# Kernel optimization log

Hardware: AMD Instinct MI355X
Metric: run time of the kernel (lower is better)

The kernel has to match this reference:

```python
import jax, jax.numpy as jnp
import numpy as np

VOCAB = 14
EMBED = 10
HIDDEN = 50
MLP = 50
PAD_IDX = 0
BATCH = 4096
SEQ = 2048


def setup_inputs() -> dict:
    key = jax.random.key(0)
    ks = jax.random.split(key, 10)
    tokens = jax.random.randint(ks[0], (BATCH, SEQ), 0, VOCAB, dtype=jnp.int64 if jax.config.jax_enable_x64 else jnp.int32)
    s_lstm = 1.0 / np.sqrt(HIDDEN)
    s_mlp1 = 1.0 / np.sqrt(HIDDEN)
    s_mlp2 = 1.0 / np.sqrt(MLP)
    emb = jax.random.normal(ks[1], (VOCAB, EMBED), jnp.float32)
    emb = emb.at[PAD_IDX].set(0.0)  # padding_idx row is zero in torch Embedding
    W_ih = jax.random.uniform(ks[2], (4 * HIDDEN, EMBED), jnp.float32, -s_lstm, s_lstm)
    W_hh = jax.random.uniform(ks[3], (4 * HIDDEN, HIDDEN), jnp.float32, -s_lstm, s_lstm)
    b_ih = jax.random.uniform(ks[4], (4 * HIDDEN,), jnp.float32, -s_lstm, s_lstm)
    b_hh = jax.random.uniform(ks[5], (4 * HIDDEN,), jnp.float32, -s_lstm, s_lstm)
    W1 = jax.random.uniform(ks[6], (MLP, HIDDEN), jnp.float32, -s_mlp1, s_mlp1)
    b1 = jax.random.uniform(ks[7], (MLP,), jnp.float32, -s_mlp1, s_mlp1)
    W2 = jax.random.uniform(ks[8], (1, MLP), jnp.float32, -s_mlp2, s_mlp2)
    b2 = jax.random.uniform(ks[9], (1,), jnp.float32, -s_mlp2, s_mlp2)
    return {"input": tokens, "emb": emb, "W_ih": W_ih, "W_hh": W_hh,
            "b_ih": b_ih, "b_hh": b_hh, "W1": W1, "b1": b1, "W2": W2, "b2": b2}


def reference(input, emb, W_ih, W_hh, b_ih, b_hh, W1, b1, W2, b2):
    x = emb[input]                                   # [B, T, E]
    mask = (input != PAD_IDX).astype(emb.dtype)      # [B, T]
    xs = jnp.swapaxes(x, 0, 1)                       # [T, B, E]
    ms = jnp.swapaxes(mask, 0, 1)[:, :, None]        # [T, B, 1]
    B = input.shape[0]

    def step(carry, inp):
        h, c = carry
        xt, mt = inp
        gates = xt @ W_ih.T + b_ih + h @ W_hh.T + b_hh  # [B, 4H], order i,f,g,o
        i, f, g, o = jnp.split(gates, 4, axis=-1)
        i = jax.nn.sigmoid(i)
        f = jax.nn.sigmoid(f)
        g = jnp.tanh(g)
        o = jax.nn.sigmoid(o)
        c_new = f * c + i * g
        h_new = o * jnp.tanh(c_new)
        # blend: keep old state on padded positions
        h = h_new * mt + h * (1.0 - mt)
        c = c_new * mt + c * (1.0 - mt)
        return (h, c), None

    h0 = jnp.zeros((B, HIDDEN), emb.dtype)
    c0 = jnp.zeros((B, HIDDEN), emb.dtype)
    (h, c), _ = jax.lax.scan(step, (h0, c0), (xs, ms))
    hidden = h @ W1.T + b1                            # [B, MLP]
    out = jax.nn.sigmoid(hidden @ W2.T + b2)          # [B, 1]
    return out
```

## Files before the change

### kernel.cpp

```cpp
#include <hip/hip_runtime.h>

#define BATCH 4096
#define SEQ   2048
#define EMB   10
#define HID   50
#define VOCAB 14
#define NTILE 13
#define TROW  2052

using bf16x8 = __attribute__((ext_vector_type(8))) short;
using f32x4  = __attribute__((ext_vector_type(4))) float;

__device__ __forceinline__ short f2bf(float f) {
  unsigned u = __builtin_bit_cast(unsigned, f);
  u = (u + 0x7FFFu + ((u >> 16) & 1u)) >> 16;
  return (short)u;
}
__device__ __forceinline__ float fsigm(float x) {
  return __builtin_amdgcn_rcpf(1.0f + __builtin_amdgcn_exp2f(x * -1.44269504f));
}

__global__ void prep_kernel(const float* __restrict__ emb,  const float* __restrict__ W_ih,
                            const float* __restrict__ W_hh, const float* __restrict__ b_ih,
                            const float* __restrict__ b_hh, short* __restrict__ Apack) {
  int idx = blockIdx.x * 256 + threadIdx.x;
  if (idx >= NTILE * 2 * 64 * 8) return;
  int j    = idx & 7;
  int lane = (idx >> 3) & 63;
  int kf   = (idx >> 9) & 1;
  int t    = idx >> 10;
  int m    = lane & 15;
  int q    = m >> 2, g = m & 3;
  int jh   = 13 * q + t;
  int k    = kf * 32 + (lane >> 4) * 8 + j;
  float v = 0.0f;
  if (jh < HID) {
    int R = g * HID + jh;
    float scale = (g == 2) ? -2.885390082f : -1.442695041f;
    if (k < HID) {
      v = W_hh[R * HID + k] * scale;
    } else {
      int vo = k - HID;
      float s = b_ih[R] + b_hh[R];
      for (int e = 0; e < EMB; ++e) s += emb[vo * EMB + e] * W_ih[R * EMB + e];
      v = s * scale;
    }
  }
  Apack[idx] = f2bf(v);
}

__global__ __launch_bounds__(1024, 1) void lstm_kernel(
    const int* __restrict__ tokens, const short* __restrict__ Apack,
    const float* __restrict__ W1, const float* __restrict__ b1,
    const float* __restrict__ W2, const float* __restrict__ b2,
    float* __restrict__ out) {
  __shared__ __align__(16) unsigned char toku8[16 * TROW];
  __shared__ __align__(16) short hbuf[2][16 * 64];
  __shared__ float hfin[16 * 52];
  __shared__ float mlp_hid[16 * 52];

  const int tid  = threadIdx.x;
  const int lane = tid & 63;
  const int wv   = tid >> 6;
  const int b0   = blockIdx.x * 16;
  const int bB   = lane & 15;
  const int jj   = lane >> 4;
  const bool compute = (wv < NTILE);
  const int jhw  = 13 * jj + wv;
  const bool hval = compute && (jhw < HID);

  const bool ohdut = (wv == 13 || wv == 14) && ((lane & 7) < 7);
  const int ohrow_i = (wv - 13) * 8 + (lane >> 3);
  const int ohsub   = lane & 7;

  bf16x8 Af0 = {}, Af1 = {};
  if (compute) {
    Af0 = *(const bf16x8*)(Apack + ((wv * 2 + 0) * 64 + lane) * 8);
    Af1 = *(const bf16x8*)(Apack + ((wv * 2 + 1) * 64 + lane) * 8);
  }

  for (int i = tid; i < 16 * 512; i += 1024) {
    int row = i >> 9, c4 = i & 511;
    int4 tv = *(const int4*)&tokens[(b0 + row) * SEQ + 4 * c4];
    unsigned pk = (tv.x & 0xFF) | ((tv.y & 0xFF) << 8) |
                  ((tv.z & 0xFF) << 16) | ((tv.w & 0xFF) << 24);
    *(unsigned*)&toku8[row * TROW + 4 * c4] = pk;
  }
  if (tid < 1024) hbuf[0][tid] = 0;
  __syncthreads();

  char* hb = (char*)hbuf;
  const int rb0 = bB * 128 + 16 * ((jj + bB) & 7);
  const int rb1 = bB * 128 + 16 * (((jj + 4) + bB) & 7);
  const int hwb = bB * 128 + 16 * (((jhw >> 3) + bB) & 7) + 2 * (jhw & 7);
  const int ohoct = (ohsub < 3) ? 6 : 7;
  const int ohwd  = (ohsub < 3) ? (1 + ohsub) : (ohsub - 3);
  const int ohb   = ohrow_i * 128 + 16 * ((ohoct + ohrow_i) & 7) + 4 * ohwd;
  const unsigned char* myrow = &toku8[bB * TROW];
  const unsigned char* ohrow = &toku8[ohrow_i * TROW];

  if (ohdut) {
    int tk = ohrow[0];
    unsigned wb = ((tk == 2 * ohsub) ? 0x3F80u : 0u) |
                  ((tk == 2 * ohsub + 1) ? 0x3F800000u : 0u);
    *(unsigned*)(hb + ohb) = wb;
  }

  float c0 = 0.f, h0 = 0.f;
  unsigned mp = 0, ohp = 0;
  if (ohdut) ohp = *(const unsigned*)(ohrow);

  for (int t = 0; t < SEQ; t += 16) {
#pragma unroll
    for (int u = 0; u < 16; ++u) {
      const int T  = t + u;
      const int PB = (u & 1) * 2048, PN = PB ^ 2048;
      __syncthreads();

      f32x4 acc = {0.f, 0.f, 0.f, 0.f};
      if (compute) {
        bf16x8 Bf0 = *(const bf16x8*)(hb + PB + rb0);
        bf16x8 Bf1 = *(const bf16x8*)(hb + PB + rb1);
        if ((u & 3) == 0) mp = *(const unsigned*)(myrow + T);
        acc = __builtin_amdgcn_mfma_f32_16x16x32_bf16(Af0, Bf0, acc, 0, 0, 0);
        acc = __builtin_amdgcn_mfma_f32_16x16x32_bf16(Af1, Bf1, acc, 0, 0, 0);
      }

      if (ohdut && T + 1 < SEQ) {
        int tk = (ohp >> (8 * ((u + 1) & 3))) & 0xFF;
        unsigned wb = ((tk == 2 * ohsub) ? 0x3F80u : 0u) |
                      ((tk == 2 * ohsub + 1) ? 0x3F800000u : 0u);
        *(unsigned*)(hb + PN + ohb) = wb;
        if (((u + 1) & 3) == 3 && T + 2 < SEQ)
          ohp = *(const unsigned*)(ohrow + T + 2);
      }

      if (compute) {
        float A = __builtin_amdgcn_exp2f(acc[0]);
        float B = __builtin_amdgcn_exp2f(acc[1]);
        float C = __builtin_amdgcn_exp2f(acc[2]);
        float G = __builtin_amdgcn_exp2f(acc[3]);
        float a1 = 1.0f + A, bb1 = 1.0f + B, c1 = 1.0f + C, g1 = 1.0f + G;
        float P   = a1 * c1;
        float t1  = __builtin_fmaf(-C, bb1, bb1);
        float num = __builtin_fmaf(c0, P, t1);
        float den = P * bb1;
        float cn  = num * __builtin_amdgcn_rcpf(den);
        cn = fminf(fmaxf(cn, -30.0f), 30.0f);
        float H   = __builtin_amdgcn_exp2f(cn * -2.885390082f);
        float hd  = g1 * (1.0f + H);
        float hn  = (1.0f - H) * __builtin_amdgcn_rcpf(hd);
        const bool keep = (((mp >> (8 * (u & 3))) & 0xFF) != 0);
        c0 = keep ? cn : c0;
        h0 = keep ? hn : h0;
        if (hval) *(short*)(hb + PN + hwb) = f2bf(h0);
      }
    }
  }

  if (hval) hfin[bB * 52 + jhw] = h0;
  __syncthreads();
  for (int idx = tid; idx < 16 * 64; idx += 1024) {
    int b = idx >> 6, m = idx & 63;
    if (m < HID) {
      float s = b1[m];
      for (int j2 = 0; j2 < HID; ++j2) s += hfin[b * 52 + j2] * W1[m * HID + j2];
      mlp_hid[b * 52 + m] = s;
    }
  }
  __syncthreads();
  if (tid < 16) {
    float s = b2[0];
    for (int m2 = 0; m2 < HID; ++m2) s += mlp_hid[tid * 52 + m2] * W2[m2];
    out[b0 + tid] = fsigm(s);
  }
}

extern "C" void kernel_launch(void* const* d_in, const int* in_sizes, int n_in,
                              void* d_out, int out_size, void* d_ws, size_t ws_size,
                              hipStream_t stream) {
  const int*   tokens = (const int*)  d_in[0];
  const float* emb    = (const float*)d_in[1];
  const float* W_ih   = (const float*)d_in[2];
  const float* W_hh   = (const float*)d_in[3];
  const float* b_ih   = (const float*)d_in[4];
  const float* b_hh   = (const float*)d_in[5];
  const float* W1     = (const float*)d_in[6];
  const float* b1     = (const float*)d_in[7];
  const float* W2     = (const float*)d_in[8];
  const float* b2     = (const float*)d_in[9];
  float* outp  = (float*)d_out;
  short* Apack = (short*)d_ws;

  hipLaunchKernelGGL(prep_kernel, dim3(52), dim3(256), 0, stream,
                     emb, W_ih, W_hh, b_ih, b_hh, Apack);
  hipLaunchKernelGGL(lstm_kernel, dim3(BATCH / 16), dim3(1024), 0, stream,
                     tokens, Apack, W1, b1, W2, b2, outp);
}
```

Baseline: 849.7 us.

## Halve block to 8 waves, each computing up to two hidden tiles

The block shrinks from 16 waves to 8. Waves 0-4 now each own two of the 13 hidden-unit tiles, running two MFMA pairs and two cell updates per step; waves 5-6 write the one-hot token rows straight from LDS each step. The aim is to cut the cost of the per-timestep block barrier across fewer waves and to let two blocks share a CU. The price is a longer serial chain per wave (two cell updates) and wave imbalance, since waves 5-7 do only one tile.

```diff
diff --git a/kernel.cpp b/kernel.cpp
--- a/kernel.cpp
+++ b/kernel.cpp
@@ -49,7 +49,7 @@
   Apack[idx] = f2bf(v);
 }
 
-__global__ __launch_bounds__(1024, 1) void lstm_kernel(
+__global__ __launch_bounds__(512, 1) void lstm_kernel(
     const int* __restrict__ tokens, const short* __restrict__ Apack,
     const float* __restrict__ W1, const float* __restrict__ b1,
     const float* __restrict__ W2, const float* __restrict__ b2,
@@ -65,50 +65,74 @@
   const int b0   = blockIdx.x * 16;
   const int bB   = lane & 15;
   const int jj   = lane >> 4;
-  const bool compute = (wv < NTILE);
-  const int jhw  = 13 * jj + wv;
-  const bool hval = compute && (jhw < HID);
-
-  const bool ohdut = (wv == 13 || wv == 14) && ((lane & 7) < 7);
-  const int ohrow_i = (wv - 13) * 8 + (lane >> 3);
-  const int ohsub   = lane & 7;
-
-  bf16x8 Af0 = {}, Af1 = {};
-  if (compute) {
-    Af0 = *(const bf16x8*)(Apack + ((wv * 2 + 0) * 64 + lane) * 8);
-    Af1 = *(const bf16x8*)(Apack + ((wv * 2 + 1) * 64 + lane) * 8);
-  }
-
-  for (int i = tid; i < 16 * 512; i += 1024) {
+  const bool two = (wv < 5);
+  const int jh0  = 13 * jj + wv;
+  const int jh1  = 13 * jj + wv + 8;
+  const bool hval1 = two && (jh1 < HID);
+
+  const int ohi   = (wv - 5) * 64 + lane;
+  const bool ohact = (wv == 5 || wv == 6) && (ohi < 112);
+  const int ohr   = ohi / 7;
+  const int ohsub = ohi % 7;
+  const int ohoct = (ohsub < 3) ? 6 : 7;
+  const int ohinn = (ohsub < 3) ? (4 + 4 * ohsub) : (4 * (ohsub - 3));
+  const int ohb   = ohr * 128 + 16 * ((ohoct + ohr) & 7) + ohinn;
+  const int ohv0  = 2 * ohsub, ohv1 = 2 * ohsub + 1;
+
+  bf16x8 Af00 = {}, Af01 = {}, Af10 = {}, Af11 = {};
+  Af00 = *(const bf16x8*)(Apack + ((wv * 2 + 0) * 64 + lane) * 8);
+  Af01 = *(const bf16x8*)(Apack + ((wv * 2 + 1) * 64 + lane) * 8);
+  if (two) {
+    Af10 = *(const bf16x8*)(Apack + (((wv + 8) * 2 + 0) * 64 + lane) * 8);
+    Af11 = *(const bf16x8*)(Apack + (((wv + 8) * 2 + 1) * 64 + lane) * 8);
+  }
+
+  for (int i = tid; i < 16 * 512; i += 512) {
     int row = i >> 9, c4 = i & 511;
     int4 tv = *(const int4*)&tokens[(b0 + row) * SEQ + 4 * c4];
     unsigned pk = (tv.x & 0xFF) | ((tv.y & 0xFF) << 8) |
                   ((tv.z & 0xFF) << 16) | ((tv.w & 0xFF) << 24);
     *(unsigned*)&toku8[row * TROW + 4 * c4] = pk;
   }
-  if (tid < 1024) hbuf[0][tid] = 0;
+  for (int i = tid; i < 1024; i += 512) hbuf[0][i] = 0;
   __syncthreads();
 
   char* hb = (char*)hbuf;
-  const int rb0 = bB * 128 + 16 * ((jj + bB) & 7);
-  const int rb1 = bB * 128 + 16 * (((jj + 4) + bB) & 7);
-  const int hwb = bB * 128 + 16 * (((jhw >> 3) + bB) & 7) + 2 * (jhw & 7);
-  const int ohoct = (ohsub < 3) ? 6 : 7;
-  const int ohwd  = (ohsub < 3) ? (1 + ohsub) : (ohsub - 3);
-  const int ohb   = ohrow_i * 128 + 16 * ((ohoct + ohrow_i) & 7) + 4 * ohwd;
+  const int rb0  = bB * 128 + 16 * ((jj + bB) & 7);
+  const int rb1  = bB * 128 + 16 * (((jj + 4) + bB) & 7);
+  const int hwb0 = bB * 128 + 16 * (((jh0 >> 3) + bB) & 7) + 2 * (jh0 & 7);
+  const int hwb1 = bB * 128 + 16 * (((jh1 >> 3) + bB) & 7) + 2 * (jh1 & 7);
   const unsigned char* myrow = &toku8[bB * TROW];
-  const unsigned char* ohrow = &toku8[ohrow_i * TROW];
-
-  if (ohdut) {
-    int tk = ohrow[0];
-    unsigned wb = ((tk == 2 * ohsub) ? 0x3F80u : 0u) |
-                  ((tk == 2 * ohsub + 1) ? 0x3F800000u : 0u);
+  const unsigned char* ohtok = &toku8[ohr * TROW];
+
+  if (ohact) {
+    int tk = ohtok[0];
+    unsigned wb = ((tk == ohv0) ? 0x3F80u : 0u) | ((tk == ohv1) ? 0x3F800000u : 0u);
     *(unsigned*)(hb + ohb) = wb;
   }
 
-  float c0 = 0.f, h0 = 0.f;
-  unsigned mp = 0, ohp = 0;
-  if (ohdut) ohp = *(const unsigned*)(ohrow);
+  float c0 = 0.f, h0 = 0.f, c1 = 0.f, h1 = 0.f;
+  unsigned mp = 0;
+
+#define CELL(ACC, C, H)                                                        \
+  {                                                                            \
+    float eA = __builtin_amdgcn_exp2f(ACC[0]);                                 \
+    float eB = __builtin_amdgcn_exp2f(ACC[1]);                                 \
+    float eC = __builtin_amdgcn_exp2f(ACC[2]);                                 \
+    float eG = __builtin_amdgcn_exp2f(ACC[3]);                                 \
+    float a1 = 1.0f + eA, bb1 = 1.0f + eB, cc1 = 1.0f + eC, g1 = 1.0f + eG;    \
+    float P   = a1 * cc1;                                                      \
+    float t1  = __builtin_fmaf(-eC, bb1, bb1);                                 \
+    float num = __builtin_fmaf(C, P, t1);                                      \
+    float den = P * bb1;                                                       \
+    float cn  = num * __builtin_amdgcn_rcpf(den);                              \
+    cn = fminf(fmaxf(cn, -30.0f), 30.0f);                                      \
+    float eH  = __builtin_amdgcn_exp2f(cn * -2.885390082f);                    \
+    float hd  = g1 * (1.0f + eH);                                              \
+    float hn  = (1.0f - eH) * __builtin_amdgcn_rcpf(hd);                       \
+    C = keep ? cn : C;                                                         \
+    H = keep ? hn : H;                                                         \
+  }
 
   for (int t = 0; t < SEQ; t += 16) {
 #pragma unroll
@@ -117,50 +141,41 @@
       const int PB = (u & 1) * 2048, PN = PB ^ 2048;
       __syncthreads();
 
-      f32x4 acc = {0.f, 0.f, 0.f, 0.f};
-      if (compute) {
-        bf16x8 Bf0 = *(const bf16x8*)(hb + PB + rb0);
-        bf16x8 Bf1 = *(const bf16x8*)(hb + PB + rb1);
-        if ((u & 3) == 0) mp = *(const unsigned*)(myrow + T);
-        acc = __builtin_amdgcn_mfma_f32_16x16x32_bf16(Af0, Bf0, acc, 0, 0, 0);
-        acc = __builtin_amdgcn_mfma_f32_16x16x32_bf16(Af1, Bf1, acc, 0, 0, 0);
+      bf16x8 Bf0 = *(const bf16x8*)(hb + PB + rb0);
+      bf16x8 Bf1 = *(const bf16x8*)(hb + PB + rb1);
+      if ((u & 3) == 0) mp = *(const unsigned*)(myrow + T);
+
+      f32x4 acc0 = {0.f, 0.f, 0.f, 0.f};
+      acc0 = __builtin_amdgcn_mfma_f32_16x16x32_bf16(Af00, Bf0, acc0, 0, 0, 0);
+      acc0 = __builtin_amdgcn_mfma_f32_16x16x32_bf16(Af01, Bf1, acc0, 0, 0, 0);
+      f32x4 acc1 = {0.f, 0.f, 0.f, 0.f};
+      if (two) {
+        acc1 = __builtin_amdgcn_mfma_f32_16x16x32_bf16(Af10, Bf0, acc1, 0, 0, 0);
+        acc1 = __builtin_amdgcn_mfma_f32_16x16x32_bf16(Af11, Bf1, acc1, 0, 0, 0);
       }
 
-      if (ohdut && T + 1 < SEQ) {
-        int tk = (ohp >> (8 * ((u + 1) & 3))) & 0xFF;
-        unsigned wb = ((tk == 2 * ohsub) ? 0x3F80u : 0u) |
-                      ((tk == 2 * ohsub + 1) ? 0x3F800000u : 0u);
+      if (ohact && T + 1 < SEQ) {
+        int tk = ohtok[T + 1];
+        unsigned wb = ((tk == ohv0) ? 0x3F80u : 0u) |
+                      ((tk == ohv1) ? 0x3F800000u : 0u);
         *(unsigned*)(hb + PN + ohb) = wb;
-        if (((u + 1) & 3) == 3 && T + 2 < SEQ)
-          ohp = *(const unsigned*)(ohrow + T + 2);
       }
 
-      if (compute) {
-        float A = __builtin_amdgcn_exp2f(acc[0]);
-        float B = __builtin_amdgcn_exp2f(acc[1]);
-        float C = __builtin_amdgcn_exp2f(acc[2]);
-        float G = __builtin_amdgcn_exp2f(acc[3]);
-        float a1 = 1.0f + A, bb1 = 1.0f + B, c1 = 1.0f + C, g1 = 1.0f + G;
-        float P   = a1 * c1;
-        float t1  = __builtin_fmaf(-C, bb1, bb1);
-        float num = __builtin_fmaf(c0, P, t1);
-        float den = P * bb1;
-        float cn  = num * __builtin_amdgcn_rcpf(den);
-        cn = fminf(fmaxf(cn, -30.0f), 30.0f);
-        float H   = __builtin_amdgcn_exp2f(cn * -2.885390082f);
-        float hd  = g1 * (1.0f + H);
-        float hn  = (1.0f - H) * __builtin_amdgcn_rcpf(hd);
-        const bool keep = (((mp >> (8 * (u & 3))) & 0xFF) != 0);
-        c0 = keep ? cn : c0;
-        h0 = keep ? hn : h0;
-        if (hval) *(short*)(hb + PN + hwb) = f2bf(h0);
+      const bool keep = (((mp >> (8 * (u & 3))) & 0xFF) != 0);
+      CELL(acc0, c0, h0)
+      *(short*)(hb + PN + hwb0) = f2bf(h0);
+      if (two) {
+        CELL(acc1, c1, h1)
+        if (hval1) *(short*)(hb + PN + hwb1) = f2bf(h1);
       }
     }
   }
-
-  if (hval) hfin[bB * 52 + jhw] = h0;
+#undef CELL
+
+  hfin[bB * 52 + jh0] = h0;
+  if (hval1) hfin[bB * 52 + jh1] = h1;
   __syncthreads();
-  for (int idx = tid; idx < 16 * 64; idx += 1024) {
+  for (int idx = tid; idx < 16 * 64; idx += 512) {
     int b = idx >> 6, m = idx & 63;
     if (m < HID) {
       float s = b1[m];
@@ -194,6 +209,6 @@
 
   hipLaunchKernelGGL(prep_kernel, dim3(52), dim3(256), 0, stream,
                      emb, W_ih, W_hh, b_ih, b_hh, Apack);
-  hipLaunchKernelGGL(lstm_kernel, dim3(BATCH / 16), dim3(1024), 0, stream,
+  hipLaunchKernelGGL(lstm_kernel, dim3(BATCH / 16), dim3(512), 0, stream,
                      tokens, Apack, W1, b1, W2, b2, outp);
 }
```

Result: no change. 852.1 us (+0.3%).
